# Kernel tuning notes

Measured on AMD Instinct MI355X. Metric: run time of the kernel, lower is better.

## Reference

```python
import math
import jax, jax.numpy as jnp
import numpy as np

B, CH3, T = 64, 192, 2048  # B = batch*heads, CH3 = 3*head_dim

def setup_inputs() -> dict:
    key = jax.random.key(0)
    qkv = jax.random.normal(key, (B, CH3, T), dtype=jnp.float32)
    return {"qkv": qkv}

def reference(qkv):
    ch = qkv.shape[1] // 3
    q, k, v = jnp.split(qkv, 3, axis=1)  # each [B, ch, T]
    scale = 1.0 / math.sqrt(math.sqrt(ch))
    # scores [B, T(query), S(key)]
    weight = jnp.einsum('bct,bcs->bts', q * scale, k * scale)
    weight = jax.nn.softmax(weight.astype(jnp.float32), axis=-1).astype(weight.dtype)
    return jnp.einsum('bts,bcs->bct', weight, v)
```

## Files before the change

### kernel.cpp

```cpp
#include <hip/hip_runtime.h>


#define DHEAD 64
#define TLEN  2048
#define NB    64
#define BQ    128
#define BK    64
#define LDT   65

typedef _Float16 h16x8 __attribute__((ext_vector_type(8)));
typedef _Float16 h16x4 __attribute__((ext_vector_type(4)));
typedef _Float16 h16x2 __attribute__((ext_vector_type(2)));
typedef __fp16   fp16x2 __attribute__((ext_vector_type(2)));
typedef float f32x4 __attribute__((ext_vector_type(4)));

#define QK_SCALE 0.42466090267246895f

extern "C" __device__ float __ocml_native_exp2_f32(float);

__device__ __forceinline__ h16x2 pkrtz(float a, float b) {
    union { fp16x2 f; h16x2 h; } u;
    u.f = __builtin_amdgcn_cvt_pkrtz(a, b);
    return u.h;
}

__device__ __forceinline__ int swz(int row, int col) {
    return row * 64 + (col ^ ((row & 7) << 3));
}

__global__ __launch_bounds__(256)
void prep(const float* __restrict__ qkv, _Float16* __restrict__ ws) {
    __shared__ float T32[64 * LDT];
    const int bx = blockIdx.x, b = blockIdx.y;
    const int tid = threadIdx.x;

    if (bx < 64) {
        const int tensor = bx >> 5, tile = bx & 31;
        const float* src = qkv + ((size_t)b * 3 + tensor) * DHEAD * TLEN + tile * 64;
        _Float16* dst = ws + (size_t)tensor * NB * DHEAD * TLEN
                      + (size_t)b * DHEAD * TLEN + (size_t)tile * 64 * DHEAD;
        {
            int c = tid >> 4, t4 = (tid & 15) * 4;
            #pragma unroll
            for (int rr = 0; rr < 4; ++rr, c += 16) {
                float4 f = *(const float4*)(src + c * TLEN + t4);
                T32[(t4 + 0) * LDT + c] = f.x;
                T32[(t4 + 1) * LDT + c] = f.y;
                T32[(t4 + 2) * LDT + c] = f.z;
                T32[(t4 + 3) * LDT + c] = f.w;
            }
        }
        __syncthreads();
        #pragma unroll
        for (int rep = 0; rep < 2; ++rep) {
            int idx = rep * 256 + tid;
            int t = idx >> 3, j = idx & 7;
            const float* row = &T32[t * LDT + j * 8];
            union { h16x8 v; h16x2 h[4]; } o;
            o.h[0] = pkrtz(row[0] * QK_SCALE, row[1] * QK_SCALE);
            o.h[1] = pkrtz(row[2] * QK_SCALE, row[3] * QK_SCALE);
            o.h[2] = pkrtz(row[4] * QK_SCALE, row[5] * QK_SCALE);
            o.h[3] = pkrtz(row[6] * QK_SCALE, row[7] * QK_SCALE);
            *(h16x8*)(dst + t * DHEAD + j * 8) = o.v;
        }
    } else {
        const int tile = bx - 64;
        const float* src = qkv + ((size_t)b * 3 + 2) * DHEAD * TLEN + tile * 64;
        _Float16* dst = ws + (size_t)2 * NB * DHEAD * TLEN
                      + (size_t)b * DHEAD * TLEN + tile * 64;
        int c = tid >> 3, t8 = (tid & 7) * 8;
        #pragma unroll
        for (int rr = 0; rr < 2; ++rr, c += 32) {
            float4 f0 = *(const float4*)(src + c * TLEN + t8);
            float4 f1 = *(const float4*)(src + c * TLEN + t8 + 4);
            union { h16x8 v; h16x2 h[4]; } o;
            o.h[0] = pkrtz(f0.x, f0.y);
            o.h[1] = pkrtz(f0.z, f0.w);
            o.h[2] = pkrtz(f1.x, f1.y);
            o.h[3] = pkrtz(f1.z, f1.w);
            *(h16x8*)(dst + c * TLEN + t8) = o.v;
        }
    }
}

__global__ __launch_bounds__(256, 4)
void attn(const _Float16* __restrict__ ws, float* __restrict__ out) {
    __shared__ alignas(16) _Float16 Ks[64 * 64];
    __shared__ alignas(16) _Float16 Vs[64 * 64];
    __shared__ alignas(16) _Float16 Pt[4][32 * 64];

    const int tid  = threadIdx.x;
    const int wave = tid >> 6;
    const int lane = tid & 63;
    const int quad = lane >> 4;
    const int c16  = lane & 15;

    const int b  = blockIdx.y;
    const int t0 = blockIdx.x * BQ;

    const _Float16* qt = ws + (size_t)b * DHEAD * TLEN + (size_t)(t0 + wave * 32) * DHEAD;
    const _Float16* kt = ws + (size_t)NB * DHEAD * TLEN + (size_t)b * DHEAD * TLEN;
    const _Float16* vd = ws + (size_t)2 * NB * DHEAD * TLEN + (size_t)b * DHEAD * TLEN;

    h16x8 qf[2][2];
    #pragma unroll
    for (int ts = 0; ts < 2; ++ts)
        #pragma unroll
        for (int kk = 0; kk < 2; ++kk)
            qf[ts][kk] = *(const h16x8*)(qt + (size_t)(ts * 16 + c16) * DHEAD + kk * 32 + quad * 8);

    f32x4 acco[4][2];
    #pragma unroll
    for (int i = 0; i < 4; ++i)
        #pragma unroll
        for (int j = 0; j < 2; ++j) acco[i][j] = f32x4{0.f, 0.f, 0.f, 0.f};
    float lp[2] = {0.f, 0.f};

    _Float16* Pw = Pt[wave];

    h16x8 kc[2], vc[2];
    #pragma unroll
    for (int r = 0; r < 2; ++r) {
        int id = tid + r * 256;
        kc[r] = *(const h16x8*)(kt + (size_t)id * 8);
        vc[r] = *(const h16x8*)(vd + (size_t)(id >> 3) * TLEN + (id & 7) * 8);
    }

    for (int it = 0; it < TLEN / BK; ++it) {
        __syncthreads();
        #pragma unroll
        for (int r = 0; r < 2; ++r) {
            int id = tid + r * 256;
            int row = id >> 3, col = (id & 7) * 8;
            *(h16x8*)(&Ks[swz(row, col)]) = kc[r];
            *(h16x8*)(&Vs[swz(row, col)]) = vc[r];
        }
        __syncthreads();

        if (it + 1 < TLEN / BK) {
            int s0 = (it + 1) * BK;
            #pragma unroll
            for (int r = 0; r < 2; ++r) {
                int id = tid + r * 256;
                kc[r] = *(const h16x8*)(kt + (size_t)s0 * DHEAD + id * 8);
                vc[r] = *(const h16x8*)(vd + (size_t)(id >> 3) * TLEN + s0 + (id & 7) * 8);
            }
        }

        f32x4 accs[4][2];
        #pragma unroll
        for (int i = 0; i < 4; ++i)
            #pragma unroll
            for (int j = 0; j < 2; ++j) accs[i][j] = f32x4{0.f, 0.f, 0.f, 0.f};
        #pragma unroll
        for (int kk = 0; kk < 2; ++kk)
            #pragma unroll
            for (int st = 0; st < 4; ++st) {
                h16x8 ka = *(const h16x8*)(&Ks[swz(st * 16 + c16, kk * 32 + quad * 8)]);
                #pragma unroll
                for (int ts = 0; ts < 2; ++ts)
                    accs[st][ts] = __builtin_amdgcn_mfma_f32_16x16x32_f16(ka, qf[ts][kk], accs[st][ts], 0, 0, 0);
            }

        #pragma unroll
        for (int st = 0; st < 4; ++st)
            #pragma unroll
            for (int ts = 0; ts < 2; ++ts) {
                f32x4 v = accs[st][ts];
                float e0 = __ocml_native_exp2_f32(v[0]);
                float e1 = __ocml_native_exp2_f32(v[1]);
                float e2 = __ocml_native_exp2_f32(v[2]);
                float e3 = __ocml_native_exp2_f32(v[3]);
                lp[ts] += (e0 + e1) + (e2 + e3);
                union { h16x4 v4; h16x2 h[2]; } p;
                p.h[0] = pkrtz(e0, e1);
                p.h[1] = pkrtz(e2, e3);
                *(h16x4*)(&Pw[swz(ts * 16 + c16, st * 16 + quad * 4)]) = p.v4;
            }

        #pragma unroll
        for (int kk = 0; kk < 2; ++kk) {
            h16x8 pb[2];
            #pragma unroll
            for (int ts = 0; ts < 2; ++ts)
                pb[ts] = *(const h16x8*)(&Pw[swz(ts * 16 + c16, kk * 32 + quad * 8)]);
            #pragma unroll
            for (int cst = 0; cst < 4; ++cst) {
                h16x8 va = *(const h16x8*)(&Vs[swz(cst * 16 + c16, kk * 32 + quad * 8)]);
                #pragma unroll
                for (int ts = 0; ts < 2; ++ts)
                    acco[cst][ts] = __builtin_amdgcn_mfma_f32_16x16x32_f16(va, pb[ts], acco[cst][ts], 0, 0, 0);
            }
        }
    }

    float rinv[2];
    #pragma unroll
    for (int ts = 0; ts < 2; ++ts) {
        float l = lp[ts];
        l += __shfl_xor(l, 16);
        l += __shfl_xor(l, 32);
        rinv[ts] = 1.0f / l;
    }

    float* ob = out + (size_t)b * DHEAD * TLEN + t0 + wave * 32;
    #pragma unroll
    for (int cst = 0; cst < 4; ++cst)
        #pragma unroll
        for (int ts = 0; ts < 2; ++ts)
            #pragma unroll
            for (int r = 0; r < 4; ++r)
                ob[(size_t)(cst * 16 + quad * 4 + r) * TLEN + ts * 16 + c16] = acco[cst][ts][r] * rinv[ts];
}

extern "C" void kernel_launch(void* const* d_in, const int* in_sizes, int n_in,
                              void* d_out, int out_size, void* d_ws, size_t ws_size,
                              hipStream_t stream) {
    const float* qkv = (const float*)d_in[0];
    _Float16* ws = (_Float16*)d_ws;
    float* out = (float*)d_out;
    prep<<<dim3(96, NB), 256, 0, stream>>>(qkv, ws);
    attn<<<dim3(TLEN / BQ, NB), 256, 0, stream>>>(ws, out);
}
```

Measured before the change: 239.8 us.

## Fuse fp16 conversion into attention kernel and switch to 32x32 MFMA tiles

Removes the separate prep kernel: Q is loaded and scaled straight from fp32 into registers, while K is staged in fp32 shared memory and transposed and converted per tile, and V is converted on load. The attention kernel moves to 32x32x16 MFMA with 64 queries per wave, uses permlane32 swaps to build P fragments in registers instead of a shared-memory round trip, adds setprio hints and remaps blocks for L2 locality. This removes the workspace write/read traffic and a launch, in exchange for per-tile conversion work, an extra barrier, and lower occupancy from more registers.

```diff
diff --git a/kernel.cpp b/kernel.cpp
--- a/kernel.cpp
+++ b/kernel.cpp
@@ -4,221 +4,212 @@
 #define DHEAD 64
 #define TLEN  2048
 #define NB    64
-#define BQ    128
+#define BQ    256
 #define BK    64
-#define LDT   65
+#define NT    (TLEN / BK)
 
 typedef _Float16 h16x8 __attribute__((ext_vector_type(8)));
-typedef _Float16 h16x4 __attribute__((ext_vector_type(4)));
 typedef _Float16 h16x2 __attribute__((ext_vector_type(2)));
 typedef __fp16   fp16x2 __attribute__((ext_vector_type(2)));
-typedef float f32x4 __attribute__((ext_vector_type(4)));
+typedef float    f32x16 __attribute__((ext_vector_type(16)));
 
 #define QK_SCALE 0.42466090267246895f
 
 extern "C" __device__ float __ocml_native_exp2_f32(float);
 
-__device__ __forceinline__ h16x2 pkrtz(float a, float b) {
-    union { fp16x2 f; h16x2 h; } u;
-    u.f = __builtin_amdgcn_cvt_pkrtz(a, b);
-    return u.h;
+union H2U  { h16x2 h; fp16x2 f; unsigned u; };
+union FRAG { h16x8 v; unsigned u[4]; };
+
+__device__ __forceinline__ unsigned pk_u(float a, float b) {
+    H2U x; x.f = __builtin_amdgcn_cvt_pkrtz(a, b); return x.u;
 }
 
 __device__ __forceinline__ int swz(int row, int col) {
     return row * 64 + (col ^ ((row & 7) << 3));
 }
-
-__global__ __launch_bounds__(256)
-void prep(const float* __restrict__ qkv, _Float16* __restrict__ ws) {
-    __shared__ float T32[64 * LDT];
-    const int bx = blockIdx.x, b = blockIdx.y;
-    const int tid = threadIdx.x;
-
-    if (bx < 64) {
-        const int tensor = bx >> 5, tile = bx & 31;
-        const float* src = qkv + ((size_t)b * 3 + tensor) * DHEAD * TLEN + tile * 64;
-        _Float16* dst = ws + (size_t)tensor * NB * DHEAD * TLEN
-                      + (size_t)b * DHEAD * TLEN + (size_t)tile * 64 * DHEAD;
-        {
-            int c = tid >> 4, t4 = (tid & 15) * 4;
-            #pragma unroll
-            for (int rr = 0; rr < 4; ++rr, c += 16) {
-                float4 f = *(const float4*)(src + c * TLEN + t4);
-                T32[(t4 + 0) * LDT + c] = f.x;
-                T32[(t4 + 1) * LDT + c] = f.y;
-                T32[(t4 + 2) * LDT + c] = f.z;
-                T32[(t4 + 3) * LDT + c] = f.w;
-            }
-        }
-        __syncthreads();
-        #pragma unroll
-        for (int rep = 0; rep < 2; ++rep) {
-            int idx = rep * 256 + tid;
-            int t = idx >> 3, j = idx & 7;
-            const float* row = &T32[t * LDT + j * 8];
-            union { h16x8 v; h16x2 h[4]; } o;
-            o.h[0] = pkrtz(row[0] * QK_SCALE, row[1] * QK_SCALE);
-            o.h[1] = pkrtz(row[2] * QK_SCALE, row[3] * QK_SCALE);
-            o.h[2] = pkrtz(row[4] * QK_SCALE, row[5] * QK_SCALE);
-            o.h[3] = pkrtz(row[6] * QK_SCALE, row[7] * QK_SCALE);
-            *(h16x8*)(dst + t * DHEAD + j * 8) = o.v;
-        }
-    } else {
-        const int tile = bx - 64;
-        const float* src = qkv + ((size_t)b * 3 + 2) * DHEAD * TLEN + tile * 64;
-        _Float16* dst = ws + (size_t)2 * NB * DHEAD * TLEN
-                      + (size_t)b * DHEAD * TLEN + tile * 64;
-        int c = tid >> 3, t8 = (tid & 7) * 8;
-        #pragma unroll
-        for (int rr = 0; rr < 2; ++rr, c += 32) {
-            float4 f0 = *(const float4*)(src + c * TLEN + t8);
-            float4 f1 = *(const float4*)(src + c * TLEN + t8 + 4);
-            union { h16x8 v; h16x2 h[4]; } o;
-            o.h[0] = pkrtz(f0.x, f0.y);
-            o.h[1] = pkrtz(f0.z, f0.w);
-            o.h[2] = pkrtz(f1.x, f1.y);
-            o.h[3] = pkrtz(f1.z, f1.w);
-            *(h16x8*)(dst + c * TLEN + t8) = o.v;
-        }
-    }
-}
-
-__global__ __launch_bounds__(256, 4)
-void attn(const _Float16* __restrict__ ws, float* __restrict__ out) {
+__device__ __forceinline__ int swzf(int c, int s) {
+    return c * 64 + (s ^ (((c >> 3) & 7) << 2));
+}
+
+__global__ __launch_bounds__(256, 2)
+void attn(const float* __restrict__ qkv, float* __restrict__ out) {
+    __shared__ alignas(16) float    Kst[64 * 64];
     __shared__ alignas(16) _Float16 Ks[64 * 64];
     __shared__ alignas(16) _Float16 Vs[64 * 64];
-    __shared__ alignas(16) _Float16 Pt[4][32 * 64];
 
     const int tid  = threadIdx.x;
     const int wave = tid >> 6;
     const int lane = tid & 63;
-    const int quad = lane >> 4;
-    const int c16  = lane & 15;
-
-    const int b  = blockIdx.y;
-    const int t0 = blockIdx.x * BQ;
-
-    const _Float16* qt = ws + (size_t)b * DHEAD * TLEN + (size_t)(t0 + wave * 32) * DHEAD;
-    const _Float16* kt = ws + (size_t)NB * DHEAD * TLEN + (size_t)b * DHEAD * TLEN;
-    const _Float16* vd = ws + (size_t)2 * NB * DHEAD * TLEN + (size_t)b * DHEAD * TLEN;
-
-    h16x8 qf[2][2];
-    #pragma unroll
-    for (int ts = 0; ts < 2; ++ts)
-        #pragma unroll
-        for (int kk = 0; kk < 2; ++kk)
-            qf[ts][kk] = *(const h16x8*)(qt + (size_t)(ts * 16 + c16) * DHEAD + kk * 32 + quad * 8);
-
-    f32x4 acco[4][2];
-    #pragma unroll
-    for (int i = 0; i < 4; ++i)
-        #pragma unroll
-        for (int j = 0; j < 2; ++j) acco[i][j] = f32x4{0.f, 0.f, 0.f, 0.f};
+    const int h    = lane >> 5;
+    const int c32  = lane & 31;
+
+    const int flat = blockIdx.x + (int)gridDim.x * blockIdx.y;
+    const int j8   = flat & 7, m8 = flat >> 3;
+    const int b    = ((m8 & 7) << 3) | j8;
+    const int t0   = (m8 >> 3) * BQ + wave * 64;
+
+    const float* qg = qkv + ((size_t)b * 3 + 0) * DHEAD * TLEN;
+    const float* kg = qkv + ((size_t)b * 3 + 1) * DHEAD * TLEN;
+    const float* vg = qkv + ((size_t)b * 3 + 2) * DHEAD * TLEN;
+
+    h16x8 qf[2][4];
+    #pragma unroll
+    for (int nb = 0; nb < 2; ++nb)
+        #pragma unroll
+        for (int kb = 0; kb < 4; ++kb) {
+            const float* qp = qg + (size_t)(kb * 16 + h * 8) * TLEN + t0 + nb * 32 + c32;
+            FRAG f;
+            #pragma unroll
+            for (int w = 0; w < 4; ++w)
+                f.u[w] = pk_u(qp[(size_t)(2 * w) * TLEN] * QK_SCALE,
+                              qp[(size_t)(2 * w + 1) * TLEN] * QK_SCALE);
+            qf[nb][kb] = f.v;
+        }
+
+    f32x16 acco[2][2];
+    #pragma unroll
+    for (int cb = 0; cb < 2; ++cb)
+        #pragma unroll
+        for (int nb = 0; nb < 2; ++nb)
+            #pragma unroll
+            for (int r = 0; r < 16; ++r) acco[cb][nb][r] = 0.f;
     float lp[2] = {0.f, 0.f};
 
-    _Float16* Pw = Pt[wave];
-
-    h16x8 kc[2], vc[2];
-    #pragma unroll
-    for (int r = 0; r < 2; ++r) {
-        int id = tid + r * 256;
-        kc[r] = *(const h16x8*)(kt + (size_t)id * 8);
-        vc[r] = *(const h16x8*)(vd + (size_t)(id >> 3) * TLEN + (id & 7) * 8);
-    }
-
-    for (int it = 0; it < TLEN / BK; ++it) {
+    const int sc = tid >> 2;
+    const int sq = (tid & 3) * 16;
+    const int ts_s   = tid >> 3;
+    const int ts_c   = (tid & 7) * 8;
+    const int ts_key = (tid & 7) << 2;
+
+    float4 kc[4];
+    h16x8  vc2[2];
+
+    auto PREF = [&](int s0) {
+        const float* kp = kg + (size_t)sc * TLEN + s0 + sq;
+        const float* vp = vg + (size_t)sc * TLEN + s0 + sq;
+        #pragma unroll
+        for (int k = 0; k < 4; ++k) kc[k] = *(const float4*)(kp + 4 * k);
+        float4 v0 = *(const float4*)(vp + 0);
+        float4 v1 = *(const float4*)(vp + 4);
+        float4 v2 = *(const float4*)(vp + 8);
+        float4 v3 = *(const float4*)(vp + 12);
+        FRAG a, c;
+        a.u[0] = pk_u(v0.x, v0.y); a.u[1] = pk_u(v0.z, v0.w);
+        a.u[2] = pk_u(v1.x, v1.y); a.u[3] = pk_u(v1.z, v1.w);
+        c.u[0] = pk_u(v2.x, v2.y); c.u[1] = pk_u(v2.z, v2.w);
+        c.u[2] = pk_u(v3.x, v3.y); c.u[3] = pk_u(v3.z, v3.w);
+        vc2[0] = a.v; vc2[1] = c.v;
+    };
+
+    PREF(0);
+
+    for (int it = 0; it < NT; ++it) {
         __syncthreads();
         #pragma unroll
-        for (int r = 0; r < 2; ++r) {
-            int id = tid + r * 256;
-            int row = id >> 3, col = (id & 7) * 8;
-            *(h16x8*)(&Ks[swz(row, col)]) = kc[r];
-            *(h16x8*)(&Vs[swz(row, col)]) = vc[r];
+        for (int k = 0; k < 4; ++k)
+            *(float4*)&Kst[swzf(sc, sq + 4 * k)] = kc[k];
+        *(h16x8*)&Vs[swz(sc, sq)]     = vc2[0];
+        *(h16x8*)&Vs[swz(sc, sq + 8)] = vc2[1];
+        __syncthreads();
+
+        if (it + 1 < NT) PREF((it + 1) * BK);
+
+        #pragma unroll
+        for (int half = 0; half < 2; ++half) {
+            const int s    = ts_s + half * 32;
+            const int scol = s ^ ts_key;
+            FRAG f;
+            #pragma unroll
+            for (int w = 0; w < 4; ++w) {
+                float f0 = Kst[(ts_c + 2 * w) * 64 + scol];
+                float f1 = Kst[(ts_c + 2 * w + 1) * 64 + scol];
+                f.u[w] = pk_u(f0 * QK_SCALE, f1 * QK_SCALE);
+            }
+            *(h16x8*)&Ks[swz(s, ts_c)] = f.v;
         }
         __syncthreads();
 
-        if (it + 1 < TLEN / BK) {
-            int s0 = (it + 1) * BK;
-            #pragma unroll
-            for (int r = 0; r < 2; ++r) {
-                int id = tid + r * 256;
-                kc[r] = *(const h16x8*)(kt + (size_t)s0 * DHEAD + id * 8);
-                vc[r] = *(const h16x8*)(vd + (size_t)(id >> 3) * TLEN + s0 + (id & 7) * 8);
-            }
-        }
-
-        f32x4 accs[4][2];
-        #pragma unroll
-        for (int i = 0; i < 4; ++i)
-            #pragma unroll
-            for (int j = 0; j < 2; ++j) accs[i][j] = f32x4{0.f, 0.f, 0.f, 0.f};
-        #pragma unroll
-        for (int kk = 0; kk < 2; ++kk)
-            #pragma unroll
-            for (int st = 0; st < 4; ++st) {
-                h16x8 ka = *(const h16x8*)(&Ks[swz(st * 16 + c16, kk * 32 + quad * 8)]);
-                #pragma unroll
-                for (int ts = 0; ts < 2; ++ts)
-                    accs[st][ts] = __builtin_amdgcn_mfma_f32_16x16x32_f16(ka, qf[ts][kk], accs[st][ts], 0, 0, 0);
-            }
-
-        #pragma unroll
-        for (int st = 0; st < 4; ++st)
-            #pragma unroll
-            for (int ts = 0; ts < 2; ++ts) {
-                f32x4 v = accs[st][ts];
-                float e0 = __ocml_native_exp2_f32(v[0]);
-                float e1 = __ocml_native_exp2_f32(v[1]);
-                float e2 = __ocml_native_exp2_f32(v[2]);
-                float e3 = __ocml_native_exp2_f32(v[3]);
-                lp[ts] += (e0 + e1) + (e2 + e3);
-                union { h16x4 v4; h16x2 h[2]; } p;
-                p.h[0] = pkrtz(e0, e1);
-                p.h[1] = pkrtz(e2, e3);
-                *(h16x4*)(&Pw[swz(ts * 16 + c16, st * 16 + quad * 4)]) = p.v4;
-            }
-
-        #pragma unroll
-        for (int kk = 0; kk < 2; ++kk) {
-            h16x8 pb[2];
-            #pragma unroll
-            for (int ts = 0; ts < 2; ++ts)
-                pb[ts] = *(const h16x8*)(&Pw[swz(ts * 16 + c16, kk * 32 + quad * 8)]);
-            #pragma unroll
-            for (int cst = 0; cst < 4; ++cst) {
-                h16x8 va = *(const h16x8*)(&Vs[swz(cst * 16 + c16, kk * 32 + quad * 8)]);
-                #pragma unroll
-                for (int ts = 0; ts < 2; ++ts)
-                    acco[cst][ts] = __builtin_amdgcn_mfma_f32_16x16x32_f16(va, pb[ts], acco[cst][ts], 0, 0, 0);
-            }
+        #pragma unroll
+        for (int mb = 0; mb < 2; ++mb) {
+            f32x16 accs[2];
+            #pragma unroll
+            for (int nb = 0; nb < 2; ++nb)
+                #pragma unroll
+                for (int r = 0; r < 16; ++r) accs[nb][r] = 0.f;
+
+            __builtin_amdgcn_s_setprio(1);
+            #pragma unroll
+            for (int kb = 0; kb < 4; ++kb) {
+                h16x8 ka = *(const h16x8*)&Ks[swz(mb * 32 + c32, kb * 16 + h * 8)];
+                accs[0] = __builtin_amdgcn_mfma_f32_32x32x16_f16(ka, qf[0][kb], accs[0], 0, 0, 0);
+                accs[1] = __builtin_amdgcn_mfma_f32_32x32x16_f16(ka, qf[1][kb], accs[1], 0, 0, 0);
+            }
+            __builtin_amdgcn_s_setprio(0);
+
+            h16x8 pb[2][2];
+            #pragma unroll
+            for (int nb = 0; nb < 2; ++nb) {
+                float e[16];
+                #pragma unroll
+                for (int r = 0; r < 16; ++r) e[r] = __ocml_native_exp2_f32(accs[nb][r]);
+                float s0 = 0.f;
+                #pragma unroll
+                for (int r = 0; r < 16; ++r) s0 += e[r];
+                lp[nb] += s0;
+                #pragma unroll
+                for (int kb16 = 0; kb16 < 2; ++kb16) {
+                    const float* ee = e + kb16 * 8;
+                    unsigned a01 = pk_u(ee[0], ee[1]);
+                    unsigned a23 = pk_u(ee[2], ee[3]);
+                    unsigned b01 = pk_u(ee[4], ee[5]);
+                    unsigned b23 = pk_u(ee[6], ee[7]);
+                    asm volatile("v_permlane32_swap_b32 %0, %1" : "+v"(a01), "+v"(b01));
+                    asm volatile("v_permlane32_swap_b32 %0, %1" : "+v"(a23), "+v"(b23));
+                    FRAG f;
+                    f.u[0] = a01; f.u[1] = a23; f.u[2] = b01; f.u[3] = b23;
+                    pb[kb16][nb] = f.v;
+                }
+            }
+
+            __builtin_amdgcn_s_setprio(1);
+            #pragma unroll
+            for (int kb16 = 0; kb16 < 2; ++kb16) {
+                const int scol = mb * 32 + kb16 * 16 + h * 8;
+                #pragma unroll
+                for (int cb = 0; cb < 2; ++cb) {
+                    h16x8 va = *(const h16x8*)&Vs[swz(cb * 32 + c32, scol)];
+                    acco[cb][0] = __builtin_amdgcn_mfma_f32_32x32x16_f16(va, pb[kb16][0], acco[cb][0], 0, 0, 0);
+                    acco[cb][1] = __builtin_amdgcn_mfma_f32_32x32x16_f16(va, pb[kb16][1], acco[cb][1], 0, 0, 0);
+                }
+            }
+            __builtin_amdgcn_s_setprio(0);
         }
     }
 
     float rinv[2];
     #pragma unroll
-    for (int ts = 0; ts < 2; ++ts) {
-        float l = lp[ts];
-        l += __shfl_xor(l, 16);
+    for (int nb = 0; nb < 2; ++nb) {
+        float l = lp[nb];
         l += __shfl_xor(l, 32);
-        rinv[ts] = 1.0f / l;
+        rinv[nb] = 1.0f / l;
     }
 
-    float* ob = out + (size_t)b * DHEAD * TLEN + t0 + wave * 32;
-    #pragma unroll
-    for (int cst = 0; cst < 4; ++cst)
-        #pragma unroll
-        for (int ts = 0; ts < 2; ++ts)
-            #pragma unroll
-            for (int r = 0; r < 4; ++r)
-                ob[(size_t)(cst * 16 + quad * 4 + r) * TLEN + ts * 16 + c16] = acco[cst][ts][r] * rinv[ts];
+    float* ob = out + (size_t)b * DHEAD * TLEN + t0;
+    #pragma unroll
+    for (int cb = 0; cb < 2; ++cb)
+        #pragma unroll
+        for (int nb = 0; nb < 2; ++nb)
+            #pragma unroll
+            for (int r = 0; r < 16; ++r) {
+                const int c = cb * 32 + (r & 3) + 8 * (r >> 2) + 4 * h;
+                ob[(size_t)c * TLEN + nb * 32 + c32] = acco[cb][nb][r] * rinv[nb];
+            }
 }
 
 extern "C" void kernel_launch(void* const* d_in, const int* in_sizes, int n_in,
                               void* d_out, int out_size, void* d_ws, size_t ws_size,
                               hipStream_t stream) {
     const float* qkv = (const float*)d_in[0];
-    _Float16* ws = (_Float16*)d_ws;
     float* out = (float*)d_out;
-    prep<<<dim3(96, NB), 256, 0, stream>>>(qkv, ws);
-    attn<<<dim3(TLEN / BQ, NB), 256, 0, stream>>>(ws, out);
-}
+    attn<<<dim3(TLEN / BQ, NB), 256, 0, stream>>>(qkv, out);
+}
```

New measurement: 242.3 us. Within noise of the previous version (+1.1%).
